# Kernel optimization log

Hardware: AMD Instinct MI355X
Metric: run time of the kernel (lower is better)

## Reference

```python
import jax, jax.numpy as jnp
import numpy as np

B, S, E, H = 4, 1024, 1024, 16
HD = E // H  # head_dim = 64


def setup_inputs() -> dict:
    key = jax.random.key(0)
    ks = jax.random.split(key, 7)
    return {
        "query": jax.random.normal(ks[0], (B, S, E), dtype=jnp.float32),
        "key": jax.random.normal(ks[1], (B, S, E), dtype=jnp.float32),
        "value": jax.random.normal(ks[2], (B, S, E), dtype=jnp.float32),
        # per-head Linear weights stacked: [H, head_dim, emb_dim] (torch Linear is y = x @ W^T)
        "Wq": jax.random.normal(ks[3], (H, HD, E), dtype=jnp.float32) * (E ** -0.5),
        "Wk": jax.random.normal(ks[4], (H, HD, E), dtype=jnp.float32) * (E ** -0.5),
        "Wv": jax.random.normal(ks[5], (H, HD, E), dtype=jnp.float32) * (E ** -0.5),
        "Wo": jax.random.normal(ks[6], (E, E), dtype=jnp.float32) * (E ** -0.5),
    }


def reference(query, key, value, Wq, Wk, Wv, Wo):
    # Project per head (all heads vectorized): [B,S,E] x [H,HD,E] -> [B,H,S,HD]
    Q = jnp.einsum('bse,hde->bhsd', query, Wq)
    K = jnp.einsum('bse,hde->bhsd', key, Wk)
    V = jnp.einsum('bse,hde->bhsd', value, Wv)
    scale = 1.0 / np.sqrt(HD)  # source divides by sqrt(emb_dim / n_head)
    scores = jnp.einsum('bhsd,bhtd->bhst', Q, K) * scale  # [B,H,S,S]
    p = jax.nn.softmax(scores, axis=-1)
    ctx = jnp.einsum('bhst,bhtd->bhsd', p, V)  # [B,H,S,HD]
    # concat heads along feature dim -> [B,S,E]
    concat = ctx.transpose(0, 2, 1, 3).reshape(query.shape[0], query.shape[1], -1)
    return concat @ Wo.T
```

## Files before the change

### kernel.cpp

```cpp
#include <hip/hip_runtime.h>

typedef __bf16 bf16_t;
typedef __bf16 bf16x4 __attribute__((ext_vector_type(4)));
typedef __bf16 bf16x8 __attribute__((ext_vector_type(8)));
typedef float f32x4 __attribute__((ext_vector_type(4)));
typedef short short4v __attribute__((ext_vector_type(4)));

#define E_DIM 1024
#define S_LEN 1024
#define NHEAD 16
#define HD_DIM 64
#define BATCH 4
#define TOKENS 4096

__device__ __forceinline__ void async_copy16(const bf16_t* g, bf16_t* l) {
    __builtin_amdgcn_global_load_lds((const __attribute__((address_space(1))) void*)g,
                                     (__attribute__((address_space(3))) void*)l,
                                     16, 0, 0);
}

__device__ __forceinline__ f32x4 pv_mfma(bf16x4 a, bf16x4 b, f32x4 c) {
#if __has_builtin(__builtin_amdgcn_mfma_f32_16x16x16_bf16)
    return __builtin_amdgcn_mfma_f32_16x16x16_bf16(a, b, c, 0, 0, 0);
#elif __has_builtin(__builtin_amdgcn_mfma_f32_16x16x16bf16_1k)
    short4v as, bs;
    __builtin_memcpy(&as, &a, 8);
    __builtin_memcpy(&bs, &b, 8);
    return __builtin_amdgcn_mfma_f32_16x16x16bf16_1k(as, bs, c, 0, 0, 0);
#else
    f32x4 d;
    asm volatile("v_mfma_f32_16x16x16_bf16 %0, %1, %2, %3\n\ts_nop 7\n\ts_nop 7"
                 : "=v"(d)
                 : "v"(a), "v"(b), "v"(c));
    return d;
#endif
}

__device__ __forceinline__ void stage_tiles(const bf16_t* gA, const bf16_t* gB,
                                            bf16_t* sAbuf, bf16_t* sBbuf,
                                            int wave, int k0) {
    const int K = 1024;
#pragma unroll
    for (int cc = 0; cc < 4; cc++) {
        int c = wave * 4 + cc;
        if (c < 8)
            async_copy16(gA + (size_t)c * 16 * K + k0, sAbuf + c * 16 * 32);
        else
            async_copy16(gB + (size_t)(c - 8) * 16 * K + k0, sBbuf + (c - 8) * 16 * 32);
    }
}

__global__ __launch_bounds__(256) void cast_all(const float* __restrict__ q,
                                                const float* __restrict__ k,
                                                const float* __restrict__ v,
                                                const float* __restrict__ wq,
                                                const float* __restrict__ wk,
                                                const float* __restrict__ wv,
                                                const float* __restrict__ wo,
                                                bf16_t* __restrict__ dst) {
    const size_t NX = (size_t)TOKENS * E_DIM;
    const size_t NW = (size_t)E_DIM * E_DIM;
    size_t i = ((size_t)blockIdx.x * 256 + threadIdx.x) * 8;
    const float* src;
    size_t off;
    if (i < 3 * NX) {
        int a = (int)(i >> 22);
        src = a == 0 ? q : (a == 1 ? k : v);
        off = i & (NX - 1);
    } else {
        size_t j = i - 3 * NX;
        int a = (int)(j >> 20);
        src = a == 0 ? wq : (a == 1 ? wk : (a == 2 ? wv : wo));
        off = j & (NW - 1);
    }
    float4 x = *(const float4*)(src + off);
    float4 y = *(const float4*)(src + off + 4);
    bf16x8 o;
    o[0] = (bf16_t)x.x; o[1] = (bf16_t)x.y; o[2] = (bf16_t)x.z; o[3] = (bf16_t)x.w;
    o[4] = (bf16_t)y.x; o[5] = (bf16_t)y.y; o[6] = (bf16_t)y.z; o[7] = (bf16_t)y.w;
    *(bf16x8*)(dst + i) = o;
}

__global__ __launch_bounds__(256, 4) void proj_gemm(const bf16_t* __restrict__ Xq,
                                                    const bf16_t* __restrict__ Xk,
                                                    const bf16_t* __restrict__ Xv,
                                                    const bf16_t* __restrict__ Wq,
                                                    const bf16_t* __restrict__ Wk,
                                                    const bf16_t* __restrict__ Wv,
                                                    bf16_t* __restrict__ Qp,
                                                    bf16_t* __restrict__ Kp,
                                                    bf16_t* __restrict__ Vp) {
    __shared__ bf16_t sA[2][128 * 32];
    __shared__ bf16_t sB[2][128 * 32];
    const int z = blockIdx.z;
    const bf16_t* A = z == 0 ? Xq : (z == 1 ? Xk : Xv);
    const bf16_t* B = z == 0 ? Wq : (z == 1 ? Wk : Wv);
    bf16_t* C = z == 0 ? Qp : (z == 1 ? Kp : Vp);
    const int N = 1024, K = 1024;
    const int lid = blockIdx.x + 8 * blockIdx.y;
    const int m0 = (((lid & 7) << 2) + ((lid >> 3) & 3)) * 128;
    const int n0 = (lid >> 5) * 128;

    const int tid = threadIdx.x;
    const int wave = tid >> 6, lane = tid & 63;
    const int quad = lane >> 4, l16 = lane & 15;
    const int wm = (wave >> 1) * 64, wn = (wave & 1) * 64;
    const int srow = lane >> 2, scol = (lane & 3) * 8;

    const bf16_t* gA = A + (size_t)(m0 + srow) * K + scol;
    const bf16_t* gB = B + (size_t)(n0 + srow) * K + scol;

    f32x4 acc[4][4];
    const f32x4 vzero = {0.f, 0.f, 0.f, 0.f};
#pragma unroll
    for (int mt = 0; mt < 4; mt++)
#pragma unroll
        for (int nt = 0; nt < 4; nt++) acc[mt][nt] = vzero;

    stage_tiles(gA, gB, sA[0], sB[0], wave, 0);
    asm volatile("s_waitcnt vmcnt(0)" ::: "memory");
    __syncthreads();

    int cur = 0;
    for (int k0 = 32; k0 < K; k0 += 32) {
        stage_tiles(gA, gB, sA[cur ^ 1], sB[cur ^ 1], wave, k0);

        bf16x8 af[4], bfr[4];
#pragma unroll
        for (int mt = 0; mt < 4; mt++)
            af[mt] = *(const bf16x8*)&sA[cur][(wm + mt * 16 + l16) * 32 + quad * 8];
#pragma unroll
        for (int nt = 0; nt < 4; nt++)
            bfr[nt] = *(const bf16x8*)&sB[cur][(wn + nt * 16 + l16) * 32 + quad * 8];
#pragma unroll
        for (int mt = 0; mt < 4; mt++)
#pragma unroll
            for (int nt = 0; nt < 4; nt++)
                acc[mt][nt] = __builtin_amdgcn_mfma_f32_16x16x32_bf16(af[mt], bfr[nt],
                                                                      acc[mt][nt], 0, 0, 0);

        asm volatile("s_waitcnt vmcnt(0)" ::: "memory");
        __syncthreads();
        cur ^= 1;
    }

    {
        bf16x8 af[4], bfr[4];
#pragma unroll
        for (int mt = 0; mt < 4; mt++)
            af[mt] = *(const bf16x8*)&sA[cur][(wm + mt * 16 + l16) * 32 + quad * 8];
#pragma unroll
        for (int nt = 0; nt < 4; nt++)
            bfr[nt] = *(const bf16x8*)&sB[cur][(wn + nt * 16 + l16) * 32 + quad * 8];
#pragma unroll
        for (int mt = 0; mt < 4; mt++)
#pragma unroll
            for (int nt = 0; nt < 4; nt++)
                acc[mt][nt] = __builtin_amdgcn_mfma_f32_16x16x32_bf16(af[mt], bfr[nt],
                                                                      acc[mt][nt], 0, 0, 0);
    }

#pragma unroll
    for (int mt = 0; mt < 4; mt++)
#pragma unroll
        for (int nt = 0; nt < 4; nt++)
#pragma unroll
            for (int r = 0; r < 4; r++) {
                int row = m0 + wm + mt * 16 + quad * 4 + r;
                int col = n0 + wn + nt * 16 + l16;
                C[(size_t)row * N + col] = (bf16_t)acc[mt][nt][r];
            }
}

__global__ __launch_bounds__(256, 4) void out_gemm(const bf16_t* __restrict__ A,
                                                   const bf16_t* __restrict__ B,
                                                   float* __restrict__ C) {
    __shared__ bf16_t sA[2][128 * 32];
    __shared__ bf16_t sB[2][128 * 32];
    const int N = 1024, K = 1024;
    const int lid = blockIdx.x + 8 * blockIdx.y;
    const int m0 = (((lid & 7) << 2) + ((lid >> 3) & 3)) * 128;
    const int n0 = (lid >> 5) * 128;

    const int tid = threadIdx.x;
    const int wave = tid >> 6, lane = tid & 63;
    const int quad = lane >> 4, l16 = lane & 15;
    const int wm = (wave >> 1) * 64, wn = (wave & 1) * 64;
    const int srow = lane >> 2, scol = (lane & 3) * 8;

    const bf16_t* gA = A + (size_t)(m0 + srow) * K + scol;
    const bf16_t* gB = B + (size_t)(n0 + srow) * K + scol;

    f32x4 acc[4][4];
    const f32x4 vzero = {0.f, 0.f, 0.f, 0.f};
#pragma unroll
    for (int mt = 0; mt < 4; mt++)
#pragma unroll
        for (int nt = 0; nt < 4; nt++) acc[mt][nt] = vzero;

    stage_tiles(gA, gB, sA[0], sB[0], wave, 0);
    asm volatile("s_waitcnt vmcnt(0)" ::: "memory");
    __syncthreads();

    int cur = 0;
    for (int k0 = 32; k0 < K; k0 += 32) {
        stage_tiles(gA, gB, sA[cur ^ 1], sB[cur ^ 1], wave, k0);

        bf16x8 af[4], bfr[4];
#pragma unroll
        for (int mt = 0; mt < 4; mt++)
            af[mt] = *(const bf16x8*)&sA[cur][(wm + mt * 16 + l16) * 32 + quad * 8];
#pragma unroll
        for (int nt = 0; nt < 4; nt++)
            bfr[nt] = *(const bf16x8*)&sB[cur][(wn + nt * 16 + l16) * 32 + quad * 8];
#pragma unroll
        for (int mt = 0; mt < 4; mt++)
#pragma unroll
            for (int nt = 0; nt < 4; nt++)
                acc[mt][nt] = __builtin_amdgcn_mfma_f32_16x16x32_bf16(af[mt], bfr[nt],
                                                                      acc[mt][nt], 0, 0, 0);

        asm volatile("s_waitcnt vmcnt(0)" ::: "memory");
        __syncthreads();
        cur ^= 1;
    }

    {
        bf16x8 af[4], bfr[4];
#pragma unroll
        for (int mt = 0; mt < 4; mt++)
            af[mt] = *(const bf16x8*)&sA[cur][(wm + mt * 16 + l16) * 32 + quad * 8];
#pragma unroll
        for (int nt = 0; nt < 4; nt++)
            bfr[nt] = *(const bf16x8*)&sB[cur][(wn + nt * 16 + l16) * 32 + quad * 8];
#pragma unroll
        for (int mt = 0; mt < 4; mt++)
#pragma unroll
            for (int nt = 0; nt < 4; nt++)
                acc[mt][nt] = __builtin_amdgcn_mfma_f32_16x16x32_bf16(af[mt], bfr[nt],
                                                                      acc[mt][nt], 0, 0, 0);
    }

#pragma unroll
    for (int mt = 0; mt < 4; mt++)
#pragma unroll
        for (int nt = 0; nt < 4; nt++)
#pragma unroll
            for (int r = 0; r < 4; r++) {
                int row = m0 + wm + mt * 16 + quad * 4 + r;
                int col = n0 + wn + nt * 16 + l16;
                C[(size_t)row * N + col] = acc[mt][nt][r];
            }
}

#define KP 72

__global__ __launch_bounds__(256, 2) void flash_attn(const bf16_t* __restrict__ Q,
                                                     const bf16_t* __restrict__ K,
                                                     const bf16_t* __restrict__ V,
                                                     bf16_t* __restrict__ O) {
    __shared__ bf16_t smem[2 * 64 * KP];
    bf16_t* sK = smem;
    bf16_t* sVt = smem + 64 * KP;

    const int tid = threadIdx.x;
    const int wave = tid >> 6, lane = tid & 63;
    const int quad = lane >> 4, l16 = lane & 15;
    const int qt = blockIdx.y >> 1;
    const int h = blockIdx.x * 2 + (blockIdx.y & 1);
    const int b = blockIdx.z;
    const size_t base = (size_t)b * S_LEN * E_DIM + h * HD_DIM;
    const float c_exp = 0.125f * 1.44269504089f;

    bf16x8 qf[2][2];
#pragma unroll
    for (int mt = 0; mt < 2; mt++) {
        const bf16_t* qp =
            Q + base + (size_t)(qt * 128 + wave * 32 + mt * 16 + l16) * E_DIM + quad * 8;
        qf[mt][0] = *(const bf16x8*)qp;
        qf[mt][1] = *(const bf16x8*)(qp + 32);
    }

    float lsum[2] = {0.f, 0.f};
    f32x4 acc[2][4];
    const f32x4 vzero = {0.f, 0.f, 0.f, 0.f};
#pragma unroll
    for (int mt = 0; mt < 2; mt++)
#pragma unroll
        for (int dt = 0; dt < 4; dt++) acc[mt][dt] = vzero;

    const int stg = tid & 7;

    for (int j0 = 0; j0 < S_LEN; j0 += 64) {
        __syncthreads();
#pragma unroll
        for (int it = 0; it < 2; it++) {
            int r = (tid >> 3) + it * 32;
            int c = stg * 8;
            bf16x8 kv = *(const bf16x8*)(K + base + (size_t)(j0 + r) * E_DIM + c);
            *(bf16x8*)&sK[r * KP + c] = kv;
            bf16x8 vv = *(const bf16x8*)(V + base + (size_t)(j0 + r) * E_DIM + c);
            int jb = (((r >> 2) ^ stg) << 2) | (r & 3);
#pragma unroll
            for (int i = 0; i < 8; i++) sVt[(c + i) * KP + jb] = vv[i];
        }
        __syncthreads();

        bf16x8 kf[4][2];
#pragma unroll
        for (int jt = 0; jt < 4; jt++) {
            kf[jt][0] = *(const bf16x8*)&sK[(jt * 16 + l16) * KP + quad * 8];
            kf[jt][1] = *(const bf16x8*)&sK[(jt * 16 + l16) * KP + 32 + quad * 8];
        }

        bf16x4 pb[2][4];
#pragma unroll
        for (int mt = 0; mt < 2; mt++)
#pragma unroll
            for (int jt = 0; jt < 4; jt++) {
                f32x4 s = vzero;
                s = __builtin_amdgcn_mfma_f32_16x16x32_bf16(kf[jt][0], qf[mt][0], s, 0, 0, 0);
                s = __builtin_amdgcn_mfma_f32_16x16x32_bf16(kf[jt][1], qf[mt][1], s, 0, 0, 0);
#pragma unroll
                for (int r = 0; r < 4; r++) {
                    float p = __builtin_amdgcn_exp2f(s[r] * c_exp);
                    lsum[mt] += p;
                    pb[mt][jt][r] = (bf16_t)p;
                }
            }

#pragma unroll
        for (int jt = 0; jt < 4; jt++)
#pragma unroll
            for (int dt = 0; dt < 4; dt++) {
                int cidx = (jt * 4 + quad) ^ (dt * 2 + (l16 >> 3));
                bf16x4 vf = *(const bf16x4*)&sVt[(dt * 16 + l16) * KP + cidx * 4];
#pragma unroll
                for (int mt = 0; mt < 2; mt++)
                    acc[mt][dt] = pv_mfma(vf, pb[mt][jt], acc[mt][dt]);
            }
    }

    float inv[2];
#pragma unroll
    for (int mt = 0; mt < 2; mt++) {
        lsum[mt] += __shfl_xor(lsum[mt], 16);
        lsum[mt] += __shfl_xor(lsum[mt], 32);
        inv[mt] = __builtin_amdgcn_rcpf(lsum[mt]);
    }

    __syncthreads();
    bf16_t* ep = smem + wave * 32 * KP;
#pragma unroll
    for (int mt = 0; mt < 2; mt++)
#pragma unroll
        for (int dt = 0; dt < 4; dt++)
#pragma unroll
            for (int r = 0; r < 4; r++)
                ep[(mt * 16 + l16) * KP + dt * 16 + quad * 4 + r] =
                    (bf16_t)(acc[mt][dt][r] * inv[mt]);
#pragma unroll
    for (int mt = 0; mt < 2; mt++)
#pragma unroll
        for (int c = 0; c < 2; c++) {
            int row = lane >> 2;
            int col = (lane & 3) * 8 + c * 32;
            bf16x8 oval = *(const bf16x8*)&ep[(mt * 16 + row) * KP + col];
            *(bf16x8*)&O[base + (size_t)(qt * 128 + wave * 32 + mt * 16 + row) * E_DIM + col] =
                oval;
        }
}

extern "C" void kernel_launch(void* const* d_in, const int* in_sizes, int n_in,
                              void* d_out, int out_size, void* d_ws, size_t ws_size,
                              hipStream_t stream) {
    const float* q  = (const float*)d_in[0];
    const float* k  = (const float*)d_in[1];
    const float* v  = (const float*)d_in[2];
    const float* wq = (const float*)d_in[3];
    const float* wk = (const float*)d_in[4];
    const float* wv = (const float*)d_in[5];
    const float* wo = (const float*)d_in[6];
    float* out = (float*)d_out;

    const int NX = TOKENS * E_DIM;
    const int NW = E_DIM * E_DIM;

    bf16_t* ws  = (bf16_t*)d_ws;
    bf16_t* Xq  = ws;
    bf16_t* Xk  = ws + (size_t)NX;
    bf16_t* Xv  = ws + (size_t)2 * NX;
    bf16_t* Wqb = ws + (size_t)3 * NX;
    bf16_t* Wkb = Wqb + NW;
    bf16_t* Wvb = Wkb + NW;
    bf16_t* Wob = Wvb + NW;
    bf16_t* Qp  = Wob + NW;
    bf16_t* Kp  = Qp + (size_t)NX;
    bf16_t* Vp  = Kp + (size_t)NX;
    bf16_t* ctx = Xq;

    cast_all<<<8192, 256, 0, stream>>>(q, k, v, wq, wk, wv, wo, Xq);

    proj_gemm<<<dim3(8, 32, 3), 256, 0, stream>>>(Xq, Xk, Xv, Wqb, Wkb, Wvb, Qp, Kp, Vp);

    flash_attn<<<dim3(8, 16, 4), 256, 0, stream>>>(Qp, Kp, Vp, ctx);

    out_gemm<<<dim3(8, 32), 256, 0, stream>>>(ctx, Wob, out);
}
```

Measured before the change: 190.8 us.

## Double-buffer K/V in flash attention and use 128x64 tiles in out GEMM

The flash attention kernel now prefetches the next K/V tile into registers while computing on the current one, then writes it into a second LDS buffer, so each iteration needs only one barrier. MFMA sections are wrapped in s_setprio to favour matrix issue. The output projection GEMM moves from 128x128 to 128x64 tiles with a custom async staging macro, doubling the block count to 512 for better CU coverage. The cost is double the LDS in attention, more register pressure, and more redundant A-tile loads in the GEMM.

```diff
diff --git a/kernel.cpp b/kernel.cpp
--- a/kernel.cpp
+++ b/kernel.cpp
@@ -176,47 +176,59 @@
                                                    const bf16_t* __restrict__ B,
                                                    float* __restrict__ C) {
     __shared__ bf16_t sA[2][128 * 32];
-    __shared__ bf16_t sB[2][128 * 32];
+    __shared__ bf16_t sB[2][64 * 32];
     const int N = 1024, K = 1024;
-    const int lid = blockIdx.x + 8 * blockIdx.y;
-    const int m0 = (((lid & 7) << 2) + ((lid >> 3) & 3)) * 128;
-    const int n0 = (lid >> 5) * 128;
+    const int wgid = blockIdx.x * 64 + blockIdx.y;
+    const int m0 = (wgid >> 4) * 128;
+    const int n0 = (wgid & 15) * 64;
 
     const int tid = threadIdx.x;
     const int wave = tid >> 6, lane = tid & 63;
     const int quad = lane >> 4, l16 = lane & 15;
-    const int wm = (wave >> 1) * 64, wn = (wave & 1) * 64;
+    const int wm = (wave >> 1) * 64, wn = (wave & 1) * 32;
     const int srow = lane >> 2, scol = (lane & 3) * 8;
 
     const bf16_t* gA = A + (size_t)(m0 + srow) * K + scol;
     const bf16_t* gB = B + (size_t)(n0 + srow) * K + scol;
 
-    f32x4 acc[4][4];
+    f32x4 acc[4][2];
     const f32x4 vzero = {0.f, 0.f, 0.f, 0.f};
 #pragma unroll
     for (int mt = 0; mt < 4; mt++)
 #pragma unroll
-        for (int nt = 0; nt < 4; nt++) acc[mt][nt] = vzero;
-
-    stage_tiles(gA, gB, sA[0], sB[0], wave, 0);
+        for (int nt = 0; nt < 2; nt++) acc[mt][nt] = vzero;
+
+#define OUT_STAGE(sa, sb, k0)                                                  \
+    {                                                                          \
+        _Pragma("unroll") for (int cc = 0; cc < 3; cc++) {                     \
+            int c = wave * 3 + cc;                                             \
+            if (c < 8)                                                         \
+                async_copy16(gA + (size_t)c * 16 * K + (k0), (sa) + c * 16 * 32); \
+            else                                                               \
+                async_copy16(gB + (size_t)(c - 8) * 16 * K + (k0),             \
+                             (sb) + (c - 8) * 16 * 32);                        \
+        }                                                                      \
+    }
+
+    OUT_STAGE(sA[0], sB[0], 0);
     asm volatile("s_waitcnt vmcnt(0)" ::: "memory");
     __syncthreads();
 
     int cur = 0;
     for (int k0 = 32; k0 < K; k0 += 32) {
-        stage_tiles(gA, gB, sA[cur ^ 1], sB[cur ^ 1], wave, k0);
-
-        bf16x8 af[4], bfr[4];
+        OUT_STAGE(sA[cur ^ 1], sB[cur ^ 1], k0);
+
+        bf16x8 af[4], bfr[2];
 #pragma unroll
         for (int mt = 0; mt < 4; mt++)
             af[mt] = *(const bf16x8*)&sA[cur][(wm + mt * 16 + l16) * 32 + quad * 8];
 #pragma unroll
-        for (int nt = 0; nt < 4; nt++)
+        for (int nt = 0; nt < 2; nt++)
             bfr[nt] = *(const bf16x8*)&sB[cur][(wn + nt * 16 + l16) * 32 + quad * 8];
 #pragma unroll
         for (int mt = 0; mt < 4; mt++)
 #pragma unroll
-            for (int nt = 0; nt < 4; nt++)
+            for (int nt = 0; nt < 2; nt++)
                 acc[mt][nt] = __builtin_amdgcn_mfma_f32_16x16x32_bf16(af[mt], bfr[nt],
                                                                       acc[mt][nt], 0, 0, 0);
 
@@ -226,17 +238,17 @@
     }
 
     {
-        bf16x8 af[4], bfr[4];
+        bf16x8 af[4], bfr[2];
 #pragma unroll
         for (int mt = 0; mt < 4; mt++)
             af[mt] = *(const bf16x8*)&sA[cur][(wm + mt * 16 + l16) * 32 + quad * 8];
 #pragma unroll
-        for (int nt = 0; nt < 4; nt++)
+        for (int nt = 0; nt < 2; nt++)
             bfr[nt] = *(const bf16x8*)&sB[cur][(wn + nt * 16 + l16) * 32 + quad * 8];
 #pragma unroll
         for (int mt = 0; mt < 4; mt++)
 #pragma unroll
-            for (int nt = 0; nt < 4; nt++)
+            for (int nt = 0; nt < 2; nt++)
                 acc[mt][nt] = __builtin_amdgcn_mfma_f32_16x16x32_bf16(af[mt], bfr[nt],
                                                                       acc[mt][nt], 0, 0, 0);
     }
@@ -244,13 +256,14 @@
 #pragma unroll
     for (int mt = 0; mt < 4; mt++)
 #pragma unroll
-        for (int nt = 0; nt < 4; nt++)
+        for (int nt = 0; nt < 2; nt++)
 #pragma unroll
             for (int r = 0; r < 4; r++) {
                 int row = m0 + wm + mt * 16 + quad * 4 + r;
                 int col = n0 + wn + nt * 16 + l16;
                 C[(size_t)row * N + col] = acc[mt][nt][r];
             }
+#undef OUT_STAGE
 }
 
 #define KP 72
@@ -259,9 +272,7 @@
                                                      const bf16_t* __restrict__ K,
                                                      const bf16_t* __restrict__ V,
                                                      bf16_t* __restrict__ O) {
-    __shared__ bf16_t smem[2 * 64 * KP];
-    bf16_t* sK = smem;
-    bf16_t* sVt = smem + 64 * KP;
+    __shared__ bf16_t smem[2][2 * 64 * KP];
 
     const int tid = threadIdx.x;
     const int wave = tid >> 6, lane = tid & 63;
@@ -290,21 +301,43 @@
         for (int dt = 0; dt < 4; dt++) acc[mt][dt] = vzero;
 
     const int stg = tid & 7;
-
+    const int r0 = tid >> 3;
+    const int c0 = stg * 8;
+    const bf16_t* Kbase = K + base + (size_t)r0 * E_DIM + c0;
+    const bf16_t* Vbase = V + base + (size_t)r0 * E_DIM + c0;
+
+    bf16x8 kvn[2], vvn[2];
+#pragma unroll
+    for (int it = 0; it < 2; it++) {
+        kvn[it] = *(const bf16x8*)(Kbase + (size_t)it * 32 * E_DIM);
+        vvn[it] = *(const bf16x8*)(Vbase + (size_t)it * 32 * E_DIM);
+    }
+    {
+        bf16_t* dK = smem[0];
+        bf16_t* dVt = smem[0] + 64 * KP;
+#pragma unroll
+        for (int it = 0; it < 2; it++) {
+            int r = r0 + it * 32;
+            *(bf16x8*)&dK[r * KP + c0] = kvn[it];
+            int jb = (((r >> 2) ^ stg) << 2) | (r & 3);
+#pragma unroll
+            for (int i = 0; i < 8; i++) dVt[(c0 + i) * KP + jb] = vvn[it][i];
+        }
+    }
+
+    int cur = 0;
     for (int j0 = 0; j0 < S_LEN; j0 += 64) {
-        __syncthreads();
-#pragma unroll
-        for (int it = 0; it < 2; it++) {
-            int r = (tid >> 3) + it * 32;
-            int c = stg * 8;
-            bf16x8 kv = *(const bf16x8*)(K + base + (size_t)(j0 + r) * E_DIM + c);
-            *(bf16x8*)&sK[r * KP + c] = kv;
-            bf16x8 vv = *(const bf16x8*)(V + base + (size_t)(j0 + r) * E_DIM + c);
-            int jb = (((r >> 2) ^ stg) << 2) | (r & 3);
-#pragma unroll
-            for (int i = 0; i < 8; i++) sVt[(c + i) * KP + jb] = vv[i];
+        const bool more = (j0 + 64 < S_LEN);
+        if (more) {
+#pragma unroll
+            for (int it = 0; it < 2; it++) {
+                kvn[it] = *(const bf16x8*)(Kbase + (size_t)(j0 + 64 + it * 32) * E_DIM);
+                vvn[it] = *(const bf16x8*)(Vbase + (size_t)(j0 + 64 + it * 32) * E_DIM);
+            }
         }
         __syncthreads();
+        const bf16_t* sK = smem[cur];
+        const bf16_t* sVt = smem[cur] + 64 * KP;
 
         bf16x8 kf[4][2];
 #pragma unroll
@@ -319,8 +352,10 @@
 #pragma unroll
             for (int jt = 0; jt < 4; jt++) {
                 f32x4 s = vzero;
+                __builtin_amdgcn_s_setprio(1);
                 s = __builtin_amdgcn_mfma_f32_16x16x32_bf16(kf[jt][0], qf[mt][0], s, 0, 0, 0);
                 s = __builtin_amdgcn_mfma_f32_16x16x32_bf16(kf[jt][1], qf[mt][1], s, 0, 0, 0);
+                __builtin_amdgcn_s_setprio(0);
 #pragma unroll
                 for (int r = 0; r < 4; r++) {
                     float p = __builtin_amdgcn_exp2f(s[r] * c_exp);
@@ -335,10 +370,26 @@
             for (int dt = 0; dt < 4; dt++) {
                 int cidx = (jt * 4 + quad) ^ (dt * 2 + (l16 >> 3));
                 bf16x4 vf = *(const bf16x4*)&sVt[(dt * 16 + l16) * KP + cidx * 4];
+                __builtin_amdgcn_s_setprio(1);
 #pragma unroll
                 for (int mt = 0; mt < 2; mt++)
                     acc[mt][dt] = pv_mfma(vf, pb[mt][jt], acc[mt][dt]);
-            }
+                __builtin_amdgcn_s_setprio(0);
+            }
+
+        if (more) {
+            bf16_t* dK = smem[cur ^ 1];
+            bf16_t* dVt = smem[cur ^ 1] + 64 * KP;
+#pragma unroll
+            for (int it = 0; it < 2; it++) {
+                int r = r0 + it * 32;
+                *(bf16x8*)&dK[r * KP + c0] = kvn[it];
+                int jb = (((r >> 2) ^ stg) << 2) | (r & 3);
+#pragma unroll
+                for (int i = 0; i < 8; i++) dVt[(c0 + i) * KP + jb] = vvn[it][i];
+            }
+        }
+        cur ^= 1;
     }
 
     float inv[2];
@@ -350,7 +401,7 @@
     }
 
     __syncthreads();
-    bf16_t* ep = smem + wave * 32 * KP;
+    bf16_t* ep = smem[0] + wave * 32 * KP;
 #pragma unroll
     for (int mt = 0; mt < 2; mt++)
 #pragma unroll
@@ -405,5 +456,5 @@
 
     flash_attn<<<dim3(8, 16, 4), 256, 0, stream>>>(Qp, Kp, Vp, ctx);
 
-    out_gemm<<<dim3(8, 32), 256, 0, stream>>>(ctx, Wob, out);
-}
+    out_gemm<<<dim3(8, 64), 256, 0, stream>>>(ctx, Wob, out);
+}
```

Measured after the change: 197.6 us. +3.6%, slower.
